# Kernel optimization log

Hardware: AMD Instinct MI355X
Metric: run time of the kernel (lower is better)

## Reference

```python
import jax, jax.numpy as jnp
import numpy as np

D = 256  # api_embed_channels
B = 8    # number of graphs
N = 128  # invoked APIs per graph (nodes); edges = N*N (fully connected incl. self-loops)
V = 10000


def setup_inputs() -> dict:
    key = jax.random.key(0)
    ks = jax.random.split(key, 12)
    s = 0.02
    return {
        "Xs": jax.random.normal(ks[0], (B, D), jnp.float32),
        "api_embeds": jax.random.normal(ks[1], (V, D), jnp.float32),
        "W1": jax.random.normal(ks[2], (2 * D, D), jnp.float32) * s,
        "b1": jnp.zeros((D,), jnp.float32),
        "W2": jax.random.normal(ks[3], (2 * D, D), jnp.float32) * s,
        "b2": jnp.zeros((D,), jnp.float32),
        "W3": jax.random.normal(ks[4], (2 * D, D), jnp.float32) * s,
        "b3": jnp.zeros((D,), jnp.float32),
        "W4": jax.random.normal(ks[5], (2 * D, 1), jnp.float32) * s,
        "b4": jnp.zeros((1,), jnp.float32),
        "invoked": jax.random.randint(ks[6], (B, N), 0, V, jnp.int32),
    }


def reference(Xs, api_embeds, W1, b1, W2, b2, W3, b3, W4, b4, invoked):
    # Gather invoked-API node features per graph: [B, N, D]
    feat = api_embeds[invoked]
    # Fully connected edge list in DGL insertion order: edge i -> (u=i//N, v=i%N).
    # src feats vary along axis 1 (u), dst feats along axis 2 (v).
    src = jnp.broadcast_to(feat[:, :, None, :], (B, N, N, D))
    dst = jnp.broadcast_to(feat[:, None, :, :], (B, N, N, D))
    # n2v_mlp1 per edge: Linear(2D -> D) on cat([src, dst])
    m = jnp.concatenate([src, dst], axis=-1) @ W1 + b1          # [B, N, N, D]
    # mean aggregation over incoming edges of dst v == mean over u (axis 1)
    e2n1 = jnp.mean(m, axis=1)                                   # [B, N, D]
    # n2n_mlp2: Linear(2D -> D) on cat([feat, e2n1])
    h = jnp.concatenate([feat, e2n1], axis=-1) @ W2 + b2         # [B, N, D]
    # n2v_mlp3 per edge: Linear(2D -> D) on cat([h_src, h_dst])
    hs = jnp.broadcast_to(h[:, :, None, :], (B, N, N, D))
    hd = jnp.broadcast_to(h[:, None, :, :], (B, N, N, D))
    ef = jnp.concatenate([hs, hd], axis=-1) @ W3 + b3            # [B, N, N, D]
    ef = ef.reshape(B, N * N, D)                                 # edge order u*N + v
    # edge_exist_mlp on cat([ef, x repeated per edge]): Linear(2D -> 1) + sigmoid
    x = jnp.broadcast_to(Xs[:, None, :], (B, N * N, D))
    logits = jnp.concatenate([ef, x], axis=-1) @ W4 + b4         # [B, N*N, 1]
    return jax.nn.sigmoid(logits)
```

## Files before the change

### kernel.cpp

```cpp
#include <hip/hip_runtime.h>


__device__ __forceinline__ float wred(float v) {
#pragma unroll
  for (int o = 32; o > 0; o >>= 1) v += __shfl_xor(v, o, 64);
  return v;
}
__device__ __forceinline__ float dot4(float4 a, float4 b) {
  return a.x * b.x + a.y * b.y + a.z * b.z + a.w * b.w;
}

__global__ __launch_bounds__(256) void k_prep1(
    const float* __restrict__ Xs, const float* __restrict__ api,
    const float* __restrict__ W3, const float* __restrict__ b3,
    const float* __restrict__ W4, const float* __restrict__ b4,
    const int* __restrict__ invoked,
    float* __restrict__ feat, float* __restrict__ wa, float* __restrict__ wb,
    float* __restrict__ c0) {
  const int blk = blockIdx.x, tid = threadIdx.x;
  const int lane = tid & 63, wv = tid >> 6;
  if (blk < 256) {
    int row = blk * 4 + wv;
    int idx = invoked[row];
    ((float4*)(feat + row * 256))[lane] =
        ((const float4*)(api + idx * 256))[lane];
  } else if (blk < 384) {
    int r = (blk - 256) * 4 + wv;
    float4 w4 = ((const float4*)W4)[lane];
    float4 rv = ((const float4*)(W3 + r * 256))[lane];
    float s = wred(dot4(rv, w4));
    if (lane == 0) { if (r < 256) wa[r] = s; else wb[r - 256] = s; }
  } else {
    float4 w4a = ((const float4*)W4)[lane];
    float4 w4b = ((const float4*)W4)[lane + 64];
    float sb3 = wred(dot4(((const float4*)b3)[lane], w4a));
    for (int bi = wv; bi < 8; bi += 4) {
      float xd = wred(dot4(((const float4*)(Xs + bi * 256))[lane], w4b));
      if (lane == 0) c0[bi] = b4[0] + sb3 + xd;
    }
  }
}

__global__ __launch_bounds__(256) void k_prep2(
    const float* __restrict__ W2, const float* __restrict__ b2,
    const float* __restrict__ wa, const float* __restrict__ wb,
    float* __restrict__ u2a, float* __restrict__ u2b,
    float* __restrict__ w2ta, float* __restrict__ w2tb,
    float* __restrict__ sP2) {
  const int blk = blockIdx.x, tid = threadIdx.x;
  const int lane = tid & 63, wv = tid >> 6;
  float4 a4 = ((const float4*)wa)[lane];
  float4 b4v = ((const float4*)wb)[lane];
  if (blk < 128) {
    int r = blk * 4 + wv;
    float4 rv = ((const float4*)(W2 + r * 256))[lane];
    float sa = wred(dot4(rv, a4));
    float sb = wred(dot4(rv, b4v));
    if (lane == 0) {
      if (r < 256) { w2ta[r] = sa; w2tb[r] = sb; }
      else         { u2a[r - 256] = sa; u2b[r - 256] = sb; }
    }
  } else if (wv == 0) {
    float4 bb = ((const float4*)b2)[lane];
    float4 s4 = make_float4(a4.x + b4v.x, a4.y + b4v.y,
                            a4.z + b4v.z, a4.w + b4v.w);
    float s = wred(dot4(bb, s4));
    if (lane == 0) *sP2 = s;
  }
}

__global__ __launch_bounds__(256) void k_prep3(
    const float* __restrict__ W1, const float* __restrict__ b1,
    const float* __restrict__ u2a, const float* __restrict__ u2b,
    const float* __restrict__ w2ta, const float* __restrict__ w2tb,
    const float* __restrict__ sP2,
    float* __restrict__ va, float* __restrict__ vb,
    float* __restrict__ qsum, float* __restrict__ sAll) {
  const int blk = blockIdx.x, tid = threadIdx.x;
  const int lane = tid & 63, wv = tid >> 6;
  float4 a4 = ((const float4*)u2a)[lane];
  float4 b4v = ((const float4*)u2b)[lane];
  if (blk < 128) {
    int t = blk * 4 + wv;
    float4 rv = ((const float4*)(W1 + t * 256))[lane];
    if (t < 256) {
      float s = wred(dot4(rv, a4) + dot4(rv, b4v));
      if (lane == 0) qsum[t] = s;
    } else {
      float sa = wred(dot4(rv, a4));
      float sb = wred(dot4(rv, b4v));
      int k = t - 256;
      if (lane == 0) { va[k] = w2ta[k] + sa; vb[k] = w2tb[k] + sb; }
    }
  } else if (wv == 0) {
    float4 bb = ((const float4*)b1)[lane];
    float s = wred(dot4(bb, a4) + dot4(bb, b4v));
    if (lane == 0) *sAll = *sP2 + s;
  }
}

__global__ __launch_bounds__(1024) void k_final(
    const float* __restrict__ feat,
    const float* __restrict__ va, const float* __restrict__ vb,
    const float* __restrict__ qsum, const float* __restrict__ sAll,
    const float* __restrict__ c0, float* __restrict__ out) {
  const int b = blockIdx.x, tid = threadIdx.x;
  const int lane = tid & 63, wv = tid >> 6;
  __shared__ float A[128], Bv[128], red[16], CbSh;
  float4 va4 = ((const float4*)va)[lane];
  float4 vb4 = ((const float4*)vb)[lane];
  float4 q4  = ((const float4*)qsum)[lane];
  float scacc = 0.f;
#pragma unroll
  for (int i = 0; i < 8; ++i) {
    int u = wv * 8 + i;
    float4 rv = ((const float4*)(feat + ((b << 7) + u) * 256))[lane];
    float sa = wred(dot4(rv, va4));
    float sb = wred(dot4(rv, vb4));
    float sc = wred(dot4(rv, q4));
    if (lane == 0) { A[u] = sa; Bv[u] = sb; }
    scacc += sc;
  }
  if (lane == 0) red[wv] = scacc;
  __syncthreads();
  if (tid == 0) {
    float s = 0.f;
#pragma unroll
    for (int i = 0; i < 16; ++i) s += red[i];
    CbSh = s * (1.f / 128.f) + sAll[0] + c0[b];
  }
  __syncthreads();
  float Cb = CbSh;
  float4* ob = (float4*)(out + (b << 14));
#pragma unroll
  for (int it = 0; it < 4; ++it) {
    int e4 = it * 1024 + tid;
    int e = e4 * 4;
    float a = A[e >> 7];
    int v0 = e & 127;
    float4 r;
    r.x = 1.f / (1.f + __expf(-(a + Bv[v0 + 0] + Cb)));
    r.y = 1.f / (1.f + __expf(-(a + Bv[v0 + 1] + Cb)));
    r.z = 1.f / (1.f + __expf(-(a + Bv[v0 + 2] + Cb)));
    r.w = 1.f / (1.f + __expf(-(a + Bv[v0 + 3] + Cb)));
    ob[e4] = r;
  }
}

extern "C" void kernel_launch(void* const* d_in, const int* in_sizes, int n_in,
                              void* d_out, int out_size, void* d_ws, size_t ws_size,
                              hipStream_t stream) {
  const float* Xs  = (const float*)d_in[0];
  const float* api = (const float*)d_in[1];
  const float* W1  = (const float*)d_in[2];
  const float* b1  = (const float*)d_in[3];
  const float* W2  = (const float*)d_in[4];
  const float* b2  = (const float*)d_in[5];
  const float* W3  = (const float*)d_in[6];
  const float* b3  = (const float*)d_in[7];
  const float* W4  = (const float*)d_in[8];
  const float* b4  = (const float*)d_in[9];
  const int* invoked = (const int*)d_in[10];
  float* out = (float*)d_out;

  float* ws   = (float*)d_ws;
  float* feat = ws;
  float* wa   = ws + 262144;
  float* wb   = ws + 262400;
  float* c0   = ws + 262656;
  float* u2a  = ws + 262664;
  float* u2b  = ws + 262920;
  float* w2ta = ws + 263176;
  float* w2tb = ws + 263432;
  float* sP2  = ws + 263688;
  float* va   = ws + 263689;
  float* vb   = ws + 263945;
  float* qsum = ws + 264201;
  float* sAll = ws + 264457;

  hipLaunchKernelGGL(k_prep1, dim3(385), dim3(256), 0, stream,
                     Xs, api, W3, b3, W4, b4, invoked, feat, wa, wb, c0);
  hipLaunchKernelGGL(k_prep2, dim3(129), dim3(256), 0, stream,
                     W2, b2, wa, wb, u2a, u2b, w2ta, w2tb, sP2);
  hipLaunchKernelGGL(k_prep3, dim3(129), dim3(256), 0, stream,
                     W1, b1, u2a, u2b, w2ta, w2tb, sP2, va, vb, qsum, sAll);
  hipLaunchKernelGGL(k_final, dim3(8), dim3(1024), 0, stream,
                     feat, va, vb, qsum, sAll, c0, out);
}
```

Baseline: 25.14 us.

## Fuse four prep/final kernels into one persistent kernel with atomic grid barriers

Merges the three weight-folding prep kernels and the final sigmoid kernel into a single launch. Stages are ordered with atomic counters and spin-waits instead of kernel boundaries, and the embedding gather overlaps the weight folding. The output work is also spread across 256 blocks instead of 8. This removes launch gaps and the round trip of gathered features through memory, but adds a memset launch and relies on all 385 blocks being co-resident, otherwise the spin barriers could deadlock.

```diff
diff --git a/kernel.cpp b/kernel.cpp
--- a/kernel.cpp
+++ b/kernel.cpp
@@ -1,5 +1,7 @@
 #include <hip/hip_runtime.h>
 
+
+#define SCOPE __HIP_MEMORY_SCOPE_AGENT
 
 __device__ __forceinline__ float wred(float v) {
 #pragma unroll
@@ -9,141 +11,154 @@
 __device__ __forceinline__ float dot4(float4 a, float4 b) {
   return a.x * b.x + a.y * b.y + a.z * b.z + a.w * b.w;
 }
+__device__ __forceinline__ void blk_signal(int* c) {
+  __syncthreads();
+  if (threadIdx.x == 0)
+    __hip_atomic_fetch_add(c, 1, __ATOMIC_RELEASE, SCOPE);
+}
+__device__ __forceinline__ void blk_wait(int* c, int target) {
+  if (threadIdx.x == 0) {
+    while (__hip_atomic_load(c, __ATOMIC_ACQUIRE, SCOPE) < target)
+      __builtin_amdgcn_s_sleep(4);
+  }
+  __syncthreads();
+}
 
-__global__ __launch_bounds__(256) void k_prep1(
+#define OFF_WA    0
+#define OFF_WB    256
+#define OFF_U2A   512
+#define OFF_U2B   768
+#define OFF_W2TA  1024
+#define OFF_W2TB  1280
+#define OFF_VA    1536
+#define OFF_VB    1792
+#define OFF_QSUM  2048
+#define OFF_CALL  2304
+#define OFF_BG    2560
+#define OFF_SC    3584
+#define OFF_SYNC  4608
+
+__global__ __launch_bounds__(256) void k_fused(
     const float* __restrict__ Xs, const float* __restrict__ api,
+    const float* __restrict__ W1, const float* __restrict__ b1,
+    const float* __restrict__ W2, const float* __restrict__ b2,
     const float* __restrict__ W3, const float* __restrict__ b3,
     const float* __restrict__ W4, const float* __restrict__ b4,
-    const int* __restrict__ invoked,
-    float* __restrict__ feat, float* __restrict__ wa, float* __restrict__ wb,
-    float* __restrict__ c0) {
+    const int* __restrict__ invoked, float* __restrict__ out,
+    float* __restrict__ ws) {
   const int blk = blockIdx.x, tid = threadIdx.x;
   const int lane = tid & 63, wv = tid >> 6;
-  if (blk < 256) {
-    int row = blk * 4 + wv;
-    int idx = invoked[row];
-    ((float4*)(feat + row * 256))[lane] =
-        ((const float4*)(api + idx * 256))[lane];
-  } else if (blk < 384) {
-    int r = (blk - 256) * 4 + wv;
-    float4 w4 = ((const float4*)W4)[lane];
-    float4 rv = ((const float4*)(W3 + r * 256))[lane];
-    float s = wred(dot4(rv, w4));
-    if (lane == 0) { if (r < 256) wa[r] = s; else wb[r - 256] = s; }
-  } else {
+
+  float* wa   = ws + OFF_WA;   float* wb   = ws + OFF_WB;
+  float* u2a  = ws + OFF_U2A;  float* u2b  = ws + OFF_U2B;
+  float* w2ta = ws + OFF_W2TA; float* w2tb = ws + OFF_W2TB;
+  float* va   = ws + OFF_VA;   float* vb   = ws + OFF_VB;
+  float* qsum = ws + OFF_QSUM; float* cAll = ws + OFF_CALL;
+  float* Bg   = ws + OFF_BG;   float* scar = ws + OFF_SC;
+  int* sync   = (int*)(ws + OFF_SYNC);
+  int* cnt1 = sync + 0; int* cnt2 = sync + 1; int* cntF = sync + 2;
+  int* gcnt = sync + 8;
+
+  __shared__ float Bsh[128];
+  __shared__ float c0sh[8];
+  __shared__ float sP2sh, sAllSh, CbSh;
+
+  if (blk < 128) {
+    const int r = blk * 4 + wv;
     float4 w4a = ((const float4*)W4)[lane];
-    float4 w4b = ((const float4*)W4)[lane + 64];
+    {
+      float4 rv = ((const float4*)(W3 + r * 256))[lane];
+      float s = wred(dot4(rv, w4a));
+      if (lane == 0) { if (r < 256) wa[r] = s; else wb[r - 256] = s; }
+    }
+    blk_signal(cnt1);
+    blk_wait(cnt1, 128);
+    {
+      float4 a4 = ((const float4*)wa)[lane];
+      float4 b4v = ((const float4*)wb)[lane];
+      float4 rv = ((const float4*)(W2 + r * 256))[lane];
+      float sa = wred(dot4(rv, a4));
+      float sb = wred(dot4(rv, b4v));
+      if (lane == 0) {
+        if (r < 256) { w2ta[r] = sa; w2tb[r] = sb; }
+        else         { u2a[r - 256] = sa; u2b[r - 256] = sb; }
+      }
+    }
+    blk_signal(cnt2);
+    blk_wait(cnt2, 128);
+    {
+      float4 a4 = ((const float4*)u2a)[lane];
+      float4 b4v = ((const float4*)u2b)[lane];
+      float4 rv = ((const float4*)(W1 + r * 256))[lane];
+      if (r < 256) {
+        float s = wred(dot4(rv, a4) + dot4(rv, b4v));
+        if (lane == 0) qsum[r] = s;
+      } else {
+        float sa = wred(dot4(rv, a4));
+        float sb = wred(dot4(rv, b4v));
+        if (lane == 0) { va[r - 256] = w2ta[r - 256] + sa;
+                         vb[r - 256] = w2tb[r - 256] + sb; }
+      }
+    }
+    blk_signal(cntF);
+  } else if (blk == 128) {
+    float4 w4a = ((const float4*)W4)[lane];
+    float4 w4b4 = ((const float4*)W4)[lane + 64];
     float sb3 = wred(dot4(((const float4*)b3)[lane], w4a));
     for (int bi = wv; bi < 8; bi += 4) {
-      float xd = wred(dot4(((const float4*)(Xs + bi * 256))[lane], w4b));
-      if (lane == 0) c0[bi] = b4[0] + sb3 + xd;
+      float xd = wred(dot4(((const float4*)(Xs + bi * 256))[lane], w4b4));
+      if (lane == 0) c0sh[bi] = b4[0] + sb3 + xd;
     }
-  }
-}
-
-__global__ __launch_bounds__(256) void k_prep2(
-    const float* __restrict__ W2, const float* __restrict__ b2,
-    const float* __restrict__ wa, const float* __restrict__ wb,
-    float* __restrict__ u2a, float* __restrict__ u2b,
-    float* __restrict__ w2ta, float* __restrict__ w2tb,
-    float* __restrict__ sP2) {
-  const int blk = blockIdx.x, tid = threadIdx.x;
-  const int lane = tid & 63, wv = tid >> 6;
-  float4 a4 = ((const float4*)wa)[lane];
-  float4 b4v = ((const float4*)wb)[lane];
-  if (blk < 128) {
-    int r = blk * 4 + wv;
-    float4 rv = ((const float4*)(W2 + r * 256))[lane];
-    float sa = wred(dot4(rv, a4));
-    float sb = wred(dot4(rv, b4v));
-    if (lane == 0) {
-      if (r < 256) { w2ta[r] = sa; w2tb[r] = sb; }
-      else         { u2a[r - 256] = sa; u2b[r - 256] = sb; }
+    blk_wait(cnt1, 128);
+    if (wv == 0) {
+      float4 a4 = ((const float4*)wa)[lane];
+      float4 b4v = ((const float4*)wb)[lane];
+      float4 s4 = make_float4(a4.x + b4v.x, a4.y + b4v.y,
+                              a4.z + b4v.z, a4.w + b4v.w);
+      float s = wred(dot4(((const float4*)b2)[lane], s4));
+      if (lane == 0) sP2sh = s;
     }
-  } else if (wv == 0) {
-    float4 bb = ((const float4*)b2)[lane];
-    float4 s4 = make_float4(a4.x + b4v.x, a4.y + b4v.y,
-                            a4.z + b4v.z, a4.w + b4v.w);
-    float s = wred(dot4(bb, s4));
-    if (lane == 0) *sP2 = s;
-  }
-}
-
-__global__ __launch_bounds__(256) void k_prep3(
-    const float* __restrict__ W1, const float* __restrict__ b1,
-    const float* __restrict__ u2a, const float* __restrict__ u2b,
-    const float* __restrict__ w2ta, const float* __restrict__ w2tb,
-    const float* __restrict__ sP2,
-    float* __restrict__ va, float* __restrict__ vb,
-    float* __restrict__ qsum, float* __restrict__ sAll) {
-  const int blk = blockIdx.x, tid = threadIdx.x;
-  const int lane = tid & 63, wv = tid >> 6;
-  float4 a4 = ((const float4*)u2a)[lane];
-  float4 b4v = ((const float4*)u2b)[lane];
-  if (blk < 128) {
-    int t = blk * 4 + wv;
-    float4 rv = ((const float4*)(W1 + t * 256))[lane];
-    if (t < 256) {
-      float s = wred(dot4(rv, a4) + dot4(rv, b4v));
-      if (lane == 0) qsum[t] = s;
-    } else {
-      float sa = wred(dot4(rv, a4));
-      float sb = wred(dot4(rv, b4v));
-      int k = t - 256;
-      if (lane == 0) { va[k] = w2ta[k] + sa; vb[k] = w2tb[k] + sb; }
+    blk_wait(cnt2, 128);
+    if (wv == 0) {
+      float4 a4 = ((const float4*)u2a)[lane];
+      float4 b4v = ((const float4*)u2b)[lane];
+      float4 s4 = make_float4(a4.x + b4v.x, a4.y + b4v.y,
+                              a4.z + b4v.z, a4.w + b4v.w);
+      float s = wred(dot4(((const float4*)b1)[lane], s4));
+      if (lane == 0) sAllSh = sP2sh + s;
     }
-  } else if (wv == 0) {
-    float4 bb = ((const float4*)b1)[lane];
-    float s = wred(dot4(bb, a4) + dot4(bb, b4v));
-    if (lane == 0) *sAll = *sP2 + s;
-  }
-}
-
-__global__ __launch_bounds__(1024) void k_final(
-    const float* __restrict__ feat,
-    const float* __restrict__ va, const float* __restrict__ vb,
-    const float* __restrict__ qsum, const float* __restrict__ sAll,
-    const float* __restrict__ c0, float* __restrict__ out) {
-  const int b = blockIdx.x, tid = threadIdx.x;
-  const int lane = tid & 63, wv = tid >> 6;
-  __shared__ float A[128], Bv[128], red[16], CbSh;
-  float4 va4 = ((const float4*)va)[lane];
-  float4 vb4 = ((const float4*)vb)[lane];
-  float4 q4  = ((const float4*)qsum)[lane];
-  float scacc = 0.f;
-#pragma unroll
-  for (int i = 0; i < 8; ++i) {
-    int u = wv * 8 + i;
-    float4 rv = ((const float4*)(feat + ((b << 7) + u) * 256))[lane];
+    __syncthreads();
+    if (tid < 8) cAll[tid] = c0sh[tid] + sAllSh;
+    blk_signal(cntF);
+  } else {
+    const int gid = blk - 129;
+    const int row = gid * 4 + wv;
+    const int g = row >> 7, u = row & 127;
+    int idx = invoked[row];
+    float4 rv = ((const float4*)(api + (size_t)idx * 256))[lane];
+    blk_wait(cntF, 129);
+    float4 va4 = ((const float4*)va)[lane];
+    float4 vb4 = ((const float4*)vb)[lane];
+    float4 q4 = ((const float4*)qsum)[lane];
     float sa = wred(dot4(rv, va4));
     float sb = wred(dot4(rv, vb4));
     float sc = wred(dot4(rv, q4));
-    if (lane == 0) { A[u] = sa; Bv[u] = sb; }
-    scacc += sc;
-  }
-  if (lane == 0) red[wv] = scacc;
-  __syncthreads();
-  if (tid == 0) {
-    float s = 0.f;
-#pragma unroll
-    for (int i = 0; i < 16; ++i) s += red[i];
-    CbSh = s * (1.f / 128.f) + sAll[0] + c0[b];
-  }
-  __syncthreads();
-  float Cb = CbSh;
-  float4* ob = (float4*)(out + (b << 14));
-#pragma unroll
-  for (int it = 0; it < 4; ++it) {
-    int e4 = it * 1024 + tid;
-    int e = e4 * 4;
-    float a = A[e >> 7];
-    int v0 = e & 127;
-    float4 r;
-    r.x = 1.f / (1.f + __expf(-(a + Bv[v0 + 0] + Cb)));
-    r.y = 1.f / (1.f + __expf(-(a + Bv[v0 + 1] + Cb)));
-    r.z = 1.f / (1.f + __expf(-(a + Bv[v0 + 2] + Cb)));
-    r.w = 1.f / (1.f + __expf(-(a + Bv[v0 + 3] + Cb)));
-    ob[e4] = r;
+    if (lane == 0) { Bg[row] = sb; scar[row] = sc; }
+    blk_signal(&gcnt[g]);
+    blk_wait(&gcnt[g], 32);
+    if (tid < 128) Bsh[tid] = Bg[(g << 7) + tid];
+    if (wv == 0) {
+      float t = scar[(g << 7) + lane] + scar[(g << 7) + 64 + lane];
+      t = wred(t);
+      if (lane == 0) CbSh = t * (1.f / 128.f) + cAll[g];
+    }
+    __syncthreads();
+    float Cb = CbSh;
+    float2* ob = (float2*)(out + (g << 14) + (u << 7));
+    float x0 = sa + Bsh[2 * lane] + Cb;
+    float x1 = sa + Bsh[2 * lane + 1] + Cb;
+    ob[lane] = make_float2(1.f / (1.f + __expf(-x0)),
+                           1.f / (1.f + __expf(-x1)));
   }
 }
 
@@ -162,28 +177,9 @@
   const float* b4  = (const float*)d_in[9];
   const int* invoked = (const int*)d_in[10];
   float* out = (float*)d_out;
+  float* ws = (float*)d_ws;
 
-  float* ws   = (float*)d_ws;
-  float* feat = ws;
-  float* wa   = ws + 262144;
-  float* wb   = ws + 262400;
-  float* c0   = ws + 262656;
-  float* u2a  = ws + 262664;
-  float* u2b  = ws + 262920;
-  float* w2ta = ws + 263176;
-  float* w2tb = ws + 263432;
-  float* sP2  = ws + 263688;
-  float* va   = ws + 263689;
-  float* vb   = ws + 263945;
-  float* qsum = ws + 264201;
-  float* sAll = ws + 264457;
-
-  hipLaunchKernelGGL(k_prep1, dim3(385), dim3(256), 0, stream,
-                     Xs, api, W3, b3, W4, b4, invoked, feat, wa, wb, c0);
-  hipLaunchKernelGGL(k_prep2, dim3(129), dim3(256), 0, stream,
-                     W2, b2, wa, wb, u2a, u2b, w2ta, w2tb, sP2);
-  hipLaunchKernelGGL(k_prep3, dim3(129), dim3(256), 0, stream,
-                     W1, b1, u2a, u2b, w2ta, w2tb, sP2, va, vb, qsum, sAll);
-  hipLaunchKernelGGL(k_final, dim3(8), dim3(1024), 0, stream,
-                     feat, va, vb, qsum, sAll, c0, out);
+  hipMemsetAsync((char*)d_ws + OFF_SYNC * sizeof(float), 0, 64, stream);
+  hipLaunchKernelGGL(k_fused, dim3(385), dim3(256), 0, stream,
+                     Xs, api, W1, b1, W2, b2, W3, b3, W4, b4, invoked, out, ws);
 }
```

After: 86.14 us. 243% more time.
